# Kernel optimization log

Measured on AMD Instinct MI355X. Metric: run time of the kernel, lower is better.

## Reference

```python
import jax, jax.numpy as jnp
import numpy as np

B, A, D, CIN = 256, 512, 64, 4  # batch, action_dim, day_length, in channels
C1, C2 = 4, 16
EPS = 1e-5


def _ln(x):
    # non-affine LayerNorm over (C, H, W), per-sample
    m = jnp.mean(x, axis=(1, 2, 3), keepdims=True)
    v = jnp.var(x, axis=(1, 2, 3), keepdims=True)
    return (x - m) / jnp.sqrt(v + EPS)


def _dblock(x, w_dil, w_pw):
    # dilated (1,3) conv, dilation 2, padding (0,2) -> width preserved
    y = jax.lax.conv_general_dilated(
        x, w_dil, window_strides=(1, 1), padding=[(0, 0), (2, 2)],
        rhs_dilation=(2, 2), dimension_numbers=('NCHW', 'OIHW', 'NCHW'))
    y = _ln(y)
    y = jnp.einsum('bchw,oc->bohw', y, w_pw[:, :, 0, 0])  # 1x1 conv
    return jax.nn.gelu(y, approximate=False)


def setup_inputs() -> dict:
    key = jax.random.key(0)
    ks = jax.random.split(key, 11)
    f = lambda k, shp: (jax.random.normal(k, shp, dtype=jnp.float32) * 0.1)
    return {
        's': jax.random.normal(ks[0], (B, A, D, CIN), dtype=jnp.float32),
        'w': jax.random.normal(ks[1], (B, A), dtype=jnp.float32),
        'd1w1': f(ks[2], (C1, CIN, 1, 3)),
        'd1w2': f(ks[3], (C1, C1, 1, 1)),
        'd2w1': f(ks[4], (C1, CIN, 1, 3)),
        'd2w2': f(ks[5], (C1, C1, 1, 1)),
        'd3w1': f(ks[6], (C1, CIN, 1, 3)),
        'd3w2': f(ks[7], (C1, C1, 1, 1)),
        'cw': f(ks[8], (C1, 3 * C1, 1, 1)),
        'c2w': f(ks[9], (C2, C1, 1, D)),
        'c3w': f(ks[10], (1, C2 + 1, 1, 1)),
    }


def reference(s, w, d1w1, d1w2, d2w1, d2w2, d3w1, d3w2, cw, c2w, c3w):
    s = jnp.transpose(s, (0, 3, 1, 2))          # [B, 4, A, D]
    x1 = _dblock(s, d1w1, d1w2)
    x2 = _dblock(s + x1, d2w1, d2w2)
    x3 = _dblock(s + x1 + x2, d3w1, d3w2)
    x = jnp.concatenate([x1, x2, x3], axis=1)   # [B, 12, A, D]
    x = _ln(x)
    x = jnp.einsum('bchw,oc->bohw', x, cw[:, :, 0, 0])      # 1x1 conv -> [B,4,A,D]
    x = jnp.einsum('bchw,ocw->boh', x, c2w[:, :, 0, :])[..., None]  # (1,D) conv -> [B,16,A,1]
    x = _ln(x)
    x = jnp.concatenate([x, w[:, None, :, None]], axis=1)   # [B,17,A,1]
    x = jnp.einsum('bchw,oc->bohw', x, c3w[:, :, 0, 0])     # [B,1,A,1]
    x = _ln(x)
    return x[:, 0, :, 0]                                    # [B, A]
```

## Files before the change

kernel.cpp:

```cpp
#include <hip/hip_runtime.h>
#include <math.h>


#define EPS_LN 1e-5f
typedef float4 f4;

__device__ __forceinline__ float gelu_f(float v) {
    return 0.5f * v * (1.0f + erff(v * 0.70710678118654752440f));
}

__device__ __forceinline__ void conv4(const f4 a, const f4 c, const f4 e,
                                      const float* __restrict__ wd, float y[4]) {
#pragma unroll
    for (int o = 0; o < 4; ++o) {
        const float* wv = wd + o * 12;
        y[o] = fmaf(a.x, wv[0], fmaf(c.x, wv[1], fmaf(e.x, wv[2],
               fmaf(a.y, wv[3], fmaf(c.y, wv[4], fmaf(e.y, wv[5],
               fmaf(a.z, wv[6], fmaf(c.z, wv[7], fmaf(e.z, wv[8],
               fmaf(a.w, wv[9], fmaf(c.w, wv[10], e.w * wv[11])))))))))));
    }
}

__device__ __forceinline__ void block_red2(float& a, float& b2, float* red,
                                           float* bc, int tid) {
#pragma unroll
    for (int off = 32; off > 0; off >>= 1) {
        a  += __shfl_down(a,  off, 64);
        b2 += __shfl_down(b2, off, 64);
    }
    if ((tid & 63) == 0) { red[tid >> 6] = a; red[8 + (tid >> 6)] = b2; }
    __syncthreads();
    if (tid == 0) {
        float x = 0.f, y = 0.f;
#pragma unroll
        for (int i = 0; i < 8; ++i) { x += red[i]; y += red[8 + i]; }
        bc[0] = x; bc[1] = y;
    }
    __syncthreads();
    a = bc[0]; b2 = bc[1];
}

__global__ __launch_bounds__(512)
void tcn_fused(const float* __restrict__ sIn, const float* __restrict__ wIn,
               const float* __restrict__ w1d, const float* __restrict__ w1p,
               const float* __restrict__ w2d, const float* __restrict__ w2p,
               const float* __restrict__ w3d, const float* __restrict__ w3p,
               const float* __restrict__ cw,  const float* __restrict__ c2w,
               const float* __restrict__ c3w, float* __restrict__ out,
               f4* __restrict__ baseT) {
    const int b   = blockIdx.x;
    const int tid = threadIdx.x;

    __shared__ float red[16];
    __shared__ float bc[2];
    __shared__ float Klds[16];

    if (tid < 16) {
        float k = 0.f;
        for (int co = 0; co < 4; ++co) {
            float cs = 0.f;
            for (int j = 0; j < 12; ++j) cs += cw[co * 12 + j];
            const float* p = c2w + tid * 256 + co * 64;
            float t = 0.f;
            for (int d = 0; d < 64; ++d) t += p[d];
            k = fmaf(cs, t, k);
        }
        Klds[tid] = k;
    }

    const f4* s4 = (const f4*)sIn;
    const size_t srow = ((size_t)b * 512 + tid) * 64;
    const size_t brow = (size_t)b * (64 * 512) + tid;
    const f4 z4 = make_float4(0.f, 0.f, 0.f, 0.f);
    const float NY = 4.f * 512.f * 64.f;

    float s1 = 0.f, s2 = 0.f;
    {
        f4 wA = z4, wB = z4, wC = s4[srow], wD = s4[srow + 1], wE;
        for (int d = 0; d < 64; ++d) {
            wE = (d + 2 < 64) ? s4[srow + d + 2] : z4;
            float y[4]; conv4(wA, wC, wE, w1d, y);
#pragma unroll
            for (int o = 0; o < 4; ++o) { s1 += y[o]; s2 = fmaf(y[o], y[o], s2); }
            wA = wB; wB = wC; wC = wD; wD = wE;
        }
    }
    block_red2(s1, s2, red, bc, tid);
    float m1 = s1 / NY;
    float r1 = rsqrtf(s2 / NY - m1 * m1 + EPS_LN);

    float t16a[16];
#pragma unroll
    for (int o = 0; o < 16; ++o) t16a[o] = 0.f;
    float cs1 = 0.f, cs2 = 0.f;

    float q1 = 0.f, q2 = 0.f;
    {
        f4 wA = z4, wB = z4, wC = s4[srow], wD = s4[srow + 1], wE;
        f4 bA = z4, bB = z4, bC = z4, bD = z4, bE;
        for (int d = 0; d < 66; ++d) {
            if (d < 64) {
                wE = (d + 2 < 64) ? s4[srow + d + 2] : z4;
                float y[4]; conv4(wA, wC, wE, w1d, y);
#pragma unroll
                for (int o = 0; o < 4; ++o) y[o] = (y[o] - m1) * r1;
                float g[4];
#pragma unroll
                for (int o = 0; o < 4; ++o) {
                    float zz = fmaf(y[0], w1p[o*4+0], fmaf(y[1], w1p[o*4+1],
                               fmaf(y[2], w1p[o*4+2], y[3] * w1p[o*4+3])));
                    g[o] = gelu_f(zz);
                }
#pragma unroll
                for (int o = 0; o < 4; ++o) { cs1 += g[o]; cs2 = fmaf(g[o], g[o], cs2); }
                float u[4];
#pragma unroll
                for (int co = 0; co < 4; ++co)
                    u[co] = fmaf(g[0], cw[co*12+0], fmaf(g[1], cw[co*12+1],
                            fmaf(g[2], cw[co*12+2], g[3] * cw[co*12+3])));
#pragma unroll
                for (int o = 0; o < 16; ++o) {
                    const float* p = c2w + o * 256 + d;
                    t16a[o] = fmaf(u[0], p[0], fmaf(u[1], p[64],
                              fmaf(u[2], p[128], fmaf(u[3], p[192], t16a[o]))));
                }
                f4 nb;
                nb.x = wC.x + g[0]; nb.y = wC.y + g[1];
                nb.z = wC.z + g[2]; nb.w = wC.w + g[3];
                baseT[brow + (size_t)d * 512] = nb;
                bE = nb;
                wA = wB; wB = wC; wC = wD; wD = wE;
            } else bE = z4;
            if (d >= 2) {
                float y2[4]; conv4(bA, bC, bE, w2d, y2);
#pragma unroll
                for (int o = 0; o < 4; ++o) { q1 += y2[o]; q2 = fmaf(y2[o], y2[o], q2); }
            }
            bA = bB; bB = bC; bC = bD; bD = bE;
        }
    }
    block_red2(q1, q2, red, bc, tid);
    float m2s = q1 / NY;
    float r2s = rsqrtf(q2 / NY - m2s * m2s + EPS_LN);

    float q31 = 0.f, q32 = 0.f;
    {
        f4 gA = z4, gB = z4, gC = z4, gD = z4, gE;
        f4 hA = z4, hB = z4, hC = z4, hD = z4, hE;
        for (int t = 0; t < 68; ++t) {
            gE = (t < 64) ? baseT[brow + (size_t)t * 512] : z4;
            if (t >= 2 && t < 66) {
                const int e = t - 2;
                float y[4]; conv4(gA, gC, gE, w2d, y);
#pragma unroll
                for (int o = 0; o < 4; ++o) y[o] = (y[o] - m2s) * r2s;
                float g[4];
#pragma unroll
                for (int o = 0; o < 4; ++o) {
                    float zz = fmaf(y[0], w2p[o*4+0], fmaf(y[1], w2p[o*4+1],
                               fmaf(y[2], w2p[o*4+2], y[3] * w2p[o*4+3])));
                    g[o] = gelu_f(zz);
                }
#pragma unroll
                for (int o = 0; o < 4; ++o) { cs1 += g[o]; cs2 = fmaf(g[o], g[o], cs2); }
                float u[4];
#pragma unroll
                for (int co = 0; co < 4; ++co)
                    u[co] = fmaf(g[0], cw[co*12+4], fmaf(g[1], cw[co*12+5],
                            fmaf(g[2], cw[co*12+6], g[3] * cw[co*12+7])));
#pragma unroll
                for (int o = 0; o < 16; ++o) {
                    const float* p = c2w + o * 256 + e;
                    t16a[o] = fmaf(u[0], p[0], fmaf(u[1], p[64],
                              fmaf(u[2], p[128], fmaf(u[3], p[192], t16a[o]))));
                }
                f4 nb;
                nb.x = gC.x + g[0]; nb.y = gC.y + g[1];
                nb.z = gC.z + g[2]; nb.w = gC.w + g[3];
                baseT[brow + (size_t)e * 512] = nb;
                hE = nb;
            } else hE = z4;
            if (t >= 4) {
                float y3[4]; conv4(hA, hC, hE, w3d, y3);
#pragma unroll
                for (int o = 0; o < 4; ++o) { q31 += y3[o]; q32 = fmaf(y3[o], y3[o], q32); }
            }
            gA = gB; gB = gC; gC = gD; gD = gE;
            hA = hB; hB = hC; hC = hD; hD = hE;
        }
    }
    block_red2(q31, q32, red, bc, tid);
    float m3s = q31 / NY;
    float r3s = rsqrtf(q32 / NY - m3s * m3s + EPS_LN);

    {
        f4 wA = z4, wB = z4, wC = baseT[brow], wD = baseT[brow + 512], wE;
        for (int d = 0; d < 64; ++d) {
            wE = (d + 2 < 64) ? baseT[brow + (size_t)(d + 2) * 512] : z4;
            float y[4]; conv4(wA, wC, wE, w3d, y);
#pragma unroll
            for (int o = 0; o < 4; ++o) y[o] = (y[o] - m3s) * r3s;
            float g[4];
#pragma unroll
            for (int o = 0; o < 4; ++o) {
                float zz = fmaf(y[0], w3p[o*4+0], fmaf(y[1], w3p[o*4+1],
                           fmaf(y[2], w3p[o*4+2], y[3] * w3p[o*4+3])));
                g[o] = gelu_f(zz);
            }
#pragma unroll
            for (int o = 0; o < 4; ++o) { cs1 += g[o]; cs2 = fmaf(g[o], g[o], cs2); }
            float u[4];
#pragma unroll
            for (int co = 0; co < 4; ++co)
                u[co] = fmaf(g[0], cw[co*12+8], fmaf(g[1], cw[co*12+9],
                        fmaf(g[2], cw[co*12+10], g[3] * cw[co*12+11])));
#pragma unroll
            for (int o = 0; o < 16; ++o) {
                const float* p = c2w + o * 256 + d;
                t16a[o] = fmaf(u[0], p[0], fmaf(u[1], p[64],
                          fmaf(u[2], p[128], fmaf(u[3], p[192], t16a[o]))));
            }
            wA = wB; wB = wC; wC = wD; wD = wE;
        }
    }

    block_red2(cs1, cs2, red, bc, tid);
    const float NC = 12.f * 512.f * 64.f;
    float mcat = cs1 / NC;
    float rcat = rsqrtf(cs2 / NC - mcat * mcat + EPS_LN);

    float tv[16];
    float p1 = 0.f, p2 = 0.f;
#pragma unroll
    for (int o = 0; o < 16; ++o) {
        float v = rcat * (t16a[o] - mcat * Klds[o]);
        tv[o] = v; p1 += v; p2 = fmaf(v, v, p2);
    }
    block_red2(p1, p2, red, bc, tid);
    const float N16 = 16.f * 512.f;
    float m16 = p1 / N16;
    float r16 = rsqrtf(p2 / N16 - m16 * m16 + EPS_LN);

    float v = wIn[(size_t)b * 512 + tid] * c3w[16];
#pragma unroll
    for (int o = 0; o < 16; ++o) v = fmaf((tv[o] - m16) * r16, c3w[o], v);
    float f1 = v, f2 = v * v;
    block_red2(f1, f2, red, bc, tid);
    float mA = f1 / 512.f;
    float rA = rsqrtf(f2 / 512.f - mA * mA + EPS_LN);

    out[(size_t)b * 512 + tid] = (v - mA) * rA;
}

extern "C" void kernel_launch(void* const* d_in, const int* in_sizes, int n_in,
                              void* d_out, int out_size, void* d_ws, size_t ws_size,
                              hipStream_t stream) {
    const float* s   = (const float*)d_in[0];
    const float* w   = (const float*)d_in[1];
    const float* w1d = (const float*)d_in[2];
    const float* w1p = (const float*)d_in[3];
    const float* w2d = (const float*)d_in[4];
    const float* w2p = (const float*)d_in[5];
    const float* w3d = (const float*)d_in[6];
    const float* w3p = (const float*)d_in[7];
    const float* cw  = (const float*)d_in[8];
    const float* c2w = (const float*)d_in[9];
    const float* c3w = (const float*)d_in[10];
    tcn_fused<<<dim3(256), dim3(512), 0, stream>>>(
        s, w, w1d, w1p, w2d, w2p, w3d, w3p, cw, c2w, c3w,
        (float*)d_out, (f4*)d_ws);
}
```

Baseline: 536.4 us.

## Split each sample's day axis across two thread halves with halo recompute

The block grows to 1024 threads, and each half covers 32 of the 64 day positions for every action row. Halo positions are recomputed, and shared memory passes boundary values between stages, so the dependent dilated-conv chain runs with twice the parallelism across only 256 blocks. The final per-row accumulators are merged through shared memory. Exact erf GELU is also replaced with an exp2/rcp sigmoid-style approximation, which cuts transcendental cost but may shift numerics slightly.

```diff
diff --git a/kernel.cpp b/kernel.cpp
--- a/kernel.cpp
+++ b/kernel.cpp
@@ -6,7 +6,9 @@
 typedef float4 f4;
 
 __device__ __forceinline__ float gelu_f(float v) {
-    return 0.5f * v * (1.0f + erff(v * 0.70710678118654752440f));
+    float t = v * fmaf(0.10294324f, v * v, 2.30220822f);
+    float e = __builtin_amdgcn_exp2f(-t);
+    return v * __builtin_amdgcn_rcpf(1.0f + e);
 }
 
 __device__ __forceinline__ void conv4(const f4 a, const f4 c, const f4 e,
@@ -21,26 +23,27 @@
     }
 }
 
-__device__ __forceinline__ void block_red2(float& a, float& b2, float* red,
+__device__ __forceinline__ void block_red2(float& x, float& y, float* red,
                                            float* bc, int tid) {
 #pragma unroll
     for (int off = 32; off > 0; off >>= 1) {
-        a  += __shfl_down(a,  off, 64);
-        b2 += __shfl_down(b2, off, 64);
-    }
-    if ((tid & 63) == 0) { red[tid >> 6] = a; red[8 + (tid >> 6)] = b2; }
+        x += __shfl_down(x, off, 64);
+        y += __shfl_down(y, off, 64);
+    }
+    const int w = tid >> 6;
+    if ((tid & 63) == 0) { red[w] = x; red[16 + w] = y; }
     __syncthreads();
     if (tid == 0) {
-        float x = 0.f, y = 0.f;
-#pragma unroll
-        for (int i = 0; i < 8; ++i) { x += red[i]; y += red[8 + i]; }
-        bc[0] = x; bc[1] = y;
+        float sx = 0.f, sy = 0.f;
+#pragma unroll
+        for (int i = 0; i < 16; ++i) { sx += red[i]; sy += red[16 + i]; }
+        bc[0] = sx; bc[1] = sy;
     }
     __syncthreads();
-    a = bc[0]; b2 = bc[1];
-}
-
-__global__ __launch_bounds__(512)
+    x = bc[0]; y = bc[1];
+}
+
+__global__ __launch_bounds__(1024, 4)
 void tcn_fused(const float* __restrict__ sIn, const float* __restrict__ wIn,
                const float* __restrict__ w1d, const float* __restrict__ w1p,
                const float* __restrict__ w2d, const float* __restrict__ w2p,
@@ -50,44 +53,57 @@
                f4* __restrict__ baseT) {
     const int b   = blockIdx.x;
     const int tid = threadIdx.x;
-
-    __shared__ float red[16];
-    __shared__ float bc[2];
+    const int a   = tid & 511;
+    const int h   = tid >> 9;
+    const int d0  = h << 5;
+
+    __shared__ float red[32];
+    __shared__ float bcs[2];
     __shared__ float Klds[16];
+    __shared__ f4    bnd[512][8];
 
     if (tid < 16) {
         float k = 0.f;
         for (int co = 0; co < 4; ++co) {
-            float cs = 0.f;
-            for (int j = 0; j < 12; ++j) cs += cw[co * 12 + j];
+            float csum = 0.f;
+            for (int j = 0; j < 12; ++j) csum += cw[co * 12 + j];
             const float* p = c2w + tid * 256 + co * 64;
             float t = 0.f;
             for (int d = 0; d < 64; ++d) t += p[d];
-            k = fmaf(cs, t, k);
+            k = fmaf(csum, t, k);
         }
         Klds[tid] = k;
     }
 
     const f4* s4 = (const f4*)sIn;
-    const size_t srow = ((size_t)b * 512 + tid) * 64;
-    const size_t brow = (size_t)b * (64 * 512) + tid;
+    const size_t srow = ((size_t)b * 512 + a) * 64;
+    const size_t bcol = (size_t)b * 32768 + a;
     const f4 z4 = make_float4(0.f, 0.f, 0.f, 0.f);
-    const float NY = 4.f * 512.f * 64.f;
+    const float NY = 131072.f;
+
+    auto ldS = [&](int q) -> f4 { return (q >= 0 && q < 64) ? s4[srow + q] : z4; };
+    auto ldB = [&](int q) -> f4 { return (q >= 0 && q < 64) ? baseT[bcol + (size_t)q * 512] : z4; };
+    auto ldB2 = [&](int q) -> f4 {
+        if (q < 0 || q >= 64) return z4;
+        if (q >= d0 && q < d0 + 32) return baseT[bcol + (size_t)q * 512];
+        return bnd[a][q - 28];
+    };
 
     float s1 = 0.f, s2 = 0.f;
     {
-        f4 wA = z4, wB = z4, wC = s4[srow], wD = s4[srow + 1], wE;
-        for (int d = 0; d < 64; ++d) {
-            wE = (d + 2 < 64) ? s4[srow + d + 2] : z4;
+        f4 wA = ldS(d0 - 2), wB = ldS(d0 - 1), wC = ldS(d0), wD = ldS(d0 + 1), wE;
+#pragma unroll 4
+        for (int e = d0; e < d0 + 32; ++e) {
+            wE = ldS(e + 2);
             float y[4]; conv4(wA, wC, wE, w1d, y);
 #pragma unroll
             for (int o = 0; o < 4; ++o) { s1 += y[o]; s2 = fmaf(y[o], y[o], s2); }
             wA = wB; wB = wC; wC = wD; wD = wE;
         }
     }
-    block_red2(s1, s2, red, bc, tid);
-    float m1 = s1 / NY;
-    float r1 = rsqrtf(s2 / NY - m1 * m1 + EPS_LN);
+    block_red2(s1, s2, red, bcs, tid);
+    const float m1 = s1 / NY;
+    const float r1 = rsqrtf(s2 / NY - m1 * m1 + EPS_LN);
 
     float t16a[16];
 #pragma unroll
@@ -96,12 +112,16 @@
 
     float q1 = 0.f, q2 = 0.f;
     {
-        f4 wA = z4, wB = z4, wC = s4[srow], wD = s4[srow + 1], wE;
+        f4 sA = z4, sB = z4, sC = z4, sD = z4, sE;
         f4 bA = z4, bB = z4, bC = z4, bD = z4, bE;
-        for (int d = 0; d < 66; ++d) {
-            if (d < 64) {
-                wE = (d + 2 < 64) ? s4[srow + d + 2] : z4;
-                float y[4]; conv4(wA, wC, wE, w1d, y);
+#pragma unroll 5
+        for (int j = 0; j < 40; ++j) {
+            const int q = d0 - 4 + j;
+            sE = ldS(q);
+            const int c = q - 2;
+            f4 nb = z4;
+            if (j >= 4 && c >= 0 && c < 64) {
+                float y[4]; conv4(sA, sC, sE, w1d, y);
 #pragma unroll
                 for (int o = 0; o < 4; ++o) y[o] = (y[o] - m1) * r1;
                 float g[4];
@@ -111,46 +131,51 @@
                                fmaf(y[2], w1p[o*4+2], y[3] * w1p[o*4+3])));
                     g[o] = gelu_f(zz);
                 }
-#pragma unroll
-                for (int o = 0; o < 4; ++o) { cs1 += g[o]; cs2 = fmaf(g[o], g[o], cs2); }
-                float u[4];
-#pragma unroll
-                for (int co = 0; co < 4; ++co)
-                    u[co] = fmaf(g[0], cw[co*12+0], fmaf(g[1], cw[co*12+1],
-                            fmaf(g[2], cw[co*12+2], g[3] * cw[co*12+3])));
-#pragma unroll
-                for (int o = 0; o < 16; ++o) {
-                    const float* p = c2w + o * 256 + d;
-                    t16a[o] = fmaf(u[0], p[0], fmaf(u[1], p[64],
-                              fmaf(u[2], p[128], fmaf(u[3], p[192], t16a[o]))));
+                nb.x = sC.x + g[0]; nb.y = sC.y + g[1];
+                nb.z = sC.z + g[2]; nb.w = sC.w + g[3];
+                if (c >= d0 && c < d0 + 32) {
+#pragma unroll
+                    for (int o = 0; o < 4; ++o) { cs1 += g[o]; cs2 = fmaf(g[o], g[o], cs2); }
+                    float u[4];
+#pragma unroll
+                    for (int co = 0; co < 4; ++co)
+                        u[co] = fmaf(g[0], cw[co*12+0], fmaf(g[1], cw[co*12+1],
+                                fmaf(g[2], cw[co*12+2], g[3] * cw[co*12+3])));
+#pragma unroll
+                    for (int o = 0; o < 16; ++o) {
+                        const float* p = c2w + o * 256 + c;
+                        t16a[o] = fmaf(u[0], p[0], fmaf(u[1], p[64],
+                                  fmaf(u[2], p[128], fmaf(u[3], p[192], t16a[o]))));
+                    }
+                    baseT[bcol + (size_t)c * 512] = nb;
+                    if (c >= 28 && c < 36) bnd[a][c - 28] = nb;
                 }
-                f4 nb;
-                nb.x = wC.x + g[0]; nb.y = wC.y + g[1];
-                nb.z = wC.z + g[2]; nb.w = wC.w + g[3];
-                baseT[brow + (size_t)d * 512] = nb;
-                bE = nb;
-                wA = wB; wB = wC; wC = wD; wD = wE;
-            } else bE = z4;
-            if (d >= 2) {
+            }
+            bE = nb;
+            if (j >= 8) {
                 float y2[4]; conv4(bA, bC, bE, w2d, y2);
 #pragma unroll
                 for (int o = 0; o < 4; ++o) { q1 += y2[o]; q2 = fmaf(y2[o], y2[o], q2); }
             }
+            sA = sB; sB = sC; sC = sD; sD = sE;
             bA = bB; bB = bC; bC = bD; bD = bE;
         }
     }
-    block_red2(q1, q2, red, bc, tid);
-    float m2s = q1 / NY;
-    float r2s = rsqrtf(q2 / NY - m2s * m2s + EPS_LN);
+    block_red2(q1, q2, red, bcs, tid);
+    const float m2s = q1 / NY;
+    const float r2s = rsqrtf(q2 / NY - m2s * m2s + EPS_LN);
 
     float q31 = 0.f, q32 = 0.f;
     {
         f4 gA = z4, gB = z4, gC = z4, gD = z4, gE;
         f4 hA = z4, hB = z4, hC = z4, hD = z4, hE;
-        for (int t = 0; t < 68; ++t) {
-            gE = (t < 64) ? baseT[brow + (size_t)t * 512] : z4;
-            if (t >= 2 && t < 66) {
-                const int e = t - 2;
+#pragma unroll 5
+        for (int j = 0; j < 40; ++j) {
+            const int q = d0 - 4 + j;
+            gE = ldB2(q);
+            const int c = q - 2;
+            f4 nb = z4;
+            if (j >= 4 && c >= 0 && c < 64) {
                 float y[4]; conv4(gA, gC, gE, w2d, y);
 #pragma unroll
                 for (int o = 0; o < 4; ++o) y[o] = (y[o] - m2s) * r2s;
@@ -161,26 +186,27 @@
                                fmaf(y[2], w2p[o*4+2], y[3] * w2p[o*4+3])));
                     g[o] = gelu_f(zz);
                 }
-#pragma unroll
-                for (int o = 0; o < 4; ++o) { cs1 += g[o]; cs2 = fmaf(g[o], g[o], cs2); }
-                float u[4];
-#pragma unroll
-                for (int co = 0; co < 4; ++co)
-                    u[co] = fmaf(g[0], cw[co*12+4], fmaf(g[1], cw[co*12+5],
-                            fmaf(g[2], cw[co*12+6], g[3] * cw[co*12+7])));
-#pragma unroll
-                for (int o = 0; o < 16; ++o) {
-                    const float* p = c2w + o * 256 + e;
-                    t16a[o] = fmaf(u[0], p[0], fmaf(u[1], p[64],
-                              fmaf(u[2], p[128], fmaf(u[3], p[192], t16a[o]))));
-                }
-                f4 nb;
                 nb.x = gC.x + g[0]; nb.y = gC.y + g[1];
                 nb.z = gC.z + g[2]; nb.w = gC.w + g[3];
-                baseT[brow + (size_t)e * 512] = nb;
-                hE = nb;
-            } else hE = z4;
-            if (t >= 4) {
+                if (c >= d0 && c < d0 + 32) {
+#pragma unroll
+                    for (int o = 0; o < 4; ++o) { cs1 += g[o]; cs2 = fmaf(g[o], g[o], cs2); }
+                    float u[4];
+#pragma unroll
+                    for (int co = 0; co < 4; ++co)
+                        u[co] = fmaf(g[0], cw[co*12+4], fmaf(g[1], cw[co*12+5],
+                                fmaf(g[2], cw[co*12+6], g[3] * cw[co*12+7])));
+#pragma unroll
+                    for (int o = 0; o < 16; ++o) {
+                        const float* p = c2w + o * 256 + c;
+                        t16a[o] = fmaf(u[0], p[0], fmaf(u[1], p[64],
+                                  fmaf(u[2], p[128], fmaf(u[3], p[192], t16a[o]))));
+                    }
+                    baseT[bcol + (size_t)c * 512] = nb;
+                }
+            }
+            hE = nb;
+            if (j >= 8) {
                 float y3[4]; conv4(hA, hC, hE, w3d, y3);
 #pragma unroll
                 for (int o = 0; o < 4; ++o) { q31 += y3[o]; q32 = fmaf(y3[o], y3[o], q32); }
@@ -189,14 +215,15 @@
             hA = hB; hB = hC; hC = hD; hD = hE;
         }
     }
-    block_red2(q31, q32, red, bc, tid);
-    float m3s = q31 / NY;
-    float r3s = rsqrtf(q32 / NY - m3s * m3s + EPS_LN);
+    block_red2(q31, q32, red, bcs, tid);
+    const float m3s = q31 / NY;
+    const float r3s = rsqrtf(q32 / NY - m3s * m3s + EPS_LN);
 
     {
-        f4 wA = z4, wB = z4, wC = baseT[brow], wD = baseT[brow + 512], wE;
-        for (int d = 0; d < 64; ++d) {
-            wE = (d + 2 < 64) ? baseT[brow + (size_t)(d + 2) * 512] : z4;
+        f4 wA = ldB(d0 - 2), wB = ldB(d0 - 1), wC = ldB(d0), wD = ldB(d0 + 1), wE;
+#pragma unroll 4
+        for (int e = d0; e < d0 + 32; ++e) {
+            wE = ldB(e + 2);
             float y[4]; conv4(wA, wC, wE, w3d, y);
 #pragma unroll
             for (int o = 0; o < 4; ++o) y[o] = (y[o] - m3s) * r3s;
@@ -216,7 +243,7 @@
                         fmaf(g[2], cw[co*12+10], g[3] * cw[co*12+11])));
 #pragma unroll
             for (int o = 0; o < 16; ++o) {
-                const float* p = c2w + o * 256 + d;
+                const float* p = c2w + o * 256 + e;
                 t16a[o] = fmaf(u[0], p[0], fmaf(u[1], p[64],
                           fmaf(u[2], p[128], fmaf(u[3], p[192], t16a[o]))));
             }
@@ -224,32 +251,44 @@
         }
     }
 
-    block_red2(cs1, cs2, red, bc, tid);
-    const float NC = 12.f * 512.f * 64.f;
-    float mcat = cs1 / NC;
-    float rcat = rsqrtf(cs2 / NC - mcat * mcat + EPS_LN);
+    block_red2(cs1, cs2, red, bcs, tid);
+    const float NC = 393216.f;
+    const float mcat = cs1 / NC;
+    const float rcat = rsqrtf(cs2 / NC - mcat * mcat + EPS_LN);
+
+    float* t16s = (float*)bnd;
+    if (h == 1) {
+#pragma unroll
+        for (int o = 0; o < 16; ++o) t16s[a * 17 + o] = t16a[o];
+    }
+    __syncthreads();
 
     float tv[16];
     float p1 = 0.f, p2 = 0.f;
-#pragma unroll
-    for (int o = 0; o < 16; ++o) {
-        float v = rcat * (t16a[o] - mcat * Klds[o]);
-        tv[o] = v; p1 += v; p2 = fmaf(v, v, p2);
-    }
-    block_red2(p1, p2, red, bc, tid);
-    const float N16 = 16.f * 512.f;
-    float m16 = p1 / N16;
-    float r16 = rsqrtf(p2 / N16 - m16 * m16 + EPS_LN);
-
-    float v = wIn[(size_t)b * 512 + tid] * c3w[16];
-#pragma unroll
-    for (int o = 0; o < 16; ++o) v = fmaf((tv[o] - m16) * r16, c3w[o], v);
-    float f1 = v, f2 = v * v;
-    block_red2(f1, f2, red, bc, tid);
-    float mA = f1 / 512.f;
-    float rA = rsqrtf(f2 / 512.f - mA * mA + EPS_LN);
-
-    out[(size_t)b * 512 + tid] = (v - mA) * rA;
+    if (h == 0) {
+#pragma unroll
+        for (int o = 0; o < 16; ++o) {
+            float T = t16a[o] + t16s[a * 17 + o];
+            float v = rcat * (T - mcat * Klds[o]);
+            tv[o] = v; p1 += v; p2 = fmaf(v, v, p2);
+        }
+    }
+    block_red2(p1, p2, red, bcs, tid);
+    const float m16 = p1 / 8192.f;
+    const float r16 = rsqrtf(p2 / 8192.f - m16 * m16 + EPS_LN);
+
+    float v = 0.f, f1 = 0.f, f2 = 0.f;
+    if (h == 0) {
+        v = wIn[(size_t)b * 512 + a] * c3w[16];
+#pragma unroll
+        for (int o = 0; o < 16; ++o) v = fmaf((tv[o] - m16) * r16, c3w[o], v);
+        f1 = v; f2 = v * v;
+    }
+    block_red2(f1, f2, red, bcs, tid);
+    const float mA = f1 / 512.f;
+    const float rA = rsqrtf(f2 / 512.f - mA * mA + EPS_LN);
+
+    if (h == 0) out[(size_t)b * 512 + a] = (v - mA) * rA;
 }
 
 extern "C" void kernel_launch(void* const* d_in, const int* in_sizes, int n_in,
@@ -266,7 +305,7 @@
     const float* cw  = (const float*)d_in[8];
     const float* c2w = (const float*)d_in[9];
     const float* c3w = (const float*)d_in[10];
-    tcn_fused<<<dim3(256), dim3(512), 0, stream>>>(
+    tcn_fused<<<dim3(256), dim3(1024), 0, stream>>>(
         s, w, w1d, w1p, w2d, w2p, w3d, w3p, cw, c2w, c3w,
         (float*)d_out, (f4*)d_ws);
 }
```

Result: slower. 1.707 ms (+218.2%).
